# Kernel optimization log

Hardware: AMD Instinct MI355X
Metric: run time of the kernel (lower is better)

The kernel has to match this reference:

```python
import jax, jax.numpy as jnp
import numpy as np

N = 100000
E = 1600000
F_IN = 128
HID = 64
N_CLASS = 40
NEG_SLOPE = 0.2


def setup_inputs() -> dict:
    key = jax.random.key(0)
    ks = jax.random.split(key, 16)
    s = lambda *sh: 1.0 / np.sqrt(sh[0])
    inp = {
        "x": jax.random.normal(ks[0], (N, F_IN), dtype=jnp.float32),
        "edge_index": jax.random.randint(ks[1], (2, E), 0, N, dtype=jnp.int64),
        "W1": jax.random.normal(ks[2], (F_IN, HID), jnp.float32) * s(F_IN),
        "b1": jnp.zeros((HID,), jnp.float32),
        "Wc0": jax.random.normal(ks[3], (HID, HID), jnp.float32) * s(HID),
        "att_src0": jax.random.normal(ks[4], (HID,), jnp.float32) * s(HID),
        "att_dst0": jax.random.normal(ks[5], (HID,), jnp.float32) * s(HID),
        "bias0": jnp.zeros((HID,), jnp.float32),
        "Wc1": jax.random.normal(ks[6], (HID, HID), jnp.float32) * s(HID),
        "att_src1": jax.random.normal(ks[7], (HID,), jnp.float32) * s(HID),
        "att_dst1": jax.random.normal(ks[8], (HID,), jnp.float32) * s(HID),
        "bias1": jnp.zeros((HID,), jnp.float32),
        "W2": jax.random.normal(ks[9], (HID, N_CLASS), jnp.float32) * s(HID),
        "b2": jnp.zeros((N_CLASS,), jnp.float32),
    }
    return inp


def gat_conv(x, src, dst, W, att_src, att_dst, bias):
    # x: [N, Fin]; src/dst: [E'] (self-loops already appended)
    h = x @ W                                   # [N, Fout]
    a_s = h @ att_src                           # [N]
    a_d = h @ att_dst                           # [N]
    e = jax.nn.leaky_relu(a_s[src] + a_d[dst], NEG_SLOPE)   # [E']
    # segment softmax over edges grouped by destination node
    e_max = jax.ops.segment_max(e, dst, num_segments=N)     # every node has a self-loop
    ex = jnp.exp(e - e_max[dst])
    denom = jax.ops.segment_sum(ex, dst, num_segments=N)
    alpha = ex / (denom[dst] + 1e-16)                        # [E']
    out = jax.ops.segment_sum(h[src] * alpha[:, None], dst, num_segments=N)
    return out + bias


def reference(x, edge_index, W1, b1, Wc0, att_src0, att_dst0, bias0,
              Wc1, att_src1, att_dst1, bias1, W2, b2):
    # eval mode: dropout_adj and feature dropout are identity
    loop = jnp.arange(N, dtype=edge_index.dtype)
    src = jnp.concatenate([edge_index[0], loop])
    dst = jnp.concatenate([edge_index[1], loop])

    h = jax.nn.relu(x @ W1 + b1)
    h = gat_conv(h, src, dst, Wc0, att_src0, att_dst0, bias0)
    h = jax.nn.relu(h)
    h = gat_conv(h, src, dst, Wc1, att_src1, att_dst1, bias1)
    logits = h @ W2 + b2
    return jax.nn.log_softmax(logits, axis=-1)
```

## Files before the change

### kernel.cpp

```cpp
#include <hip/hip_runtime.h>

#define N_NODES 100000
#define N_EDGES 1600000
#define F_IN    128
#define HID     64
#define N_CLASS 40
#define NEG_SLOPE 0.2f
#define ET (N_EDGES + N_NODES)
#define ROW_BLOCKS ((N_NODES + 63) / 64)

#define NCB   7
#define CAP1  294912
#define BPC   144
#define NFB   782
#define CAPF  2624
#define NT1   ((ET + 2047) / 2048)

typedef __attribute__((ext_vector_type(8))) short bf16x8;
typedef __attribute__((ext_vector_type(4))) float f32x4;

__device__ __forceinline__ unsigned int f2bf(float f) {
    unsigned int u = __float_as_uint(f);
    return (u + 0x7fffu + ((u >> 16) & 1u)) >> 16;
}

__global__ __launch_bounds__(256) void k_prepw(const float* __restrict__ W1,
        const float* __restrict__ Wc0, const float* __restrict__ Wc1,
        const float* __restrict__ W2,
        unsigned short* __restrict__ Wt1, unsigned short* __restrict__ Wtc0,
        unsigned short* __restrict__ Wtc1, unsigned short* __restrict__ W2t,
        int* __restrict__ zbuf, int zcount) {
    int g = blockIdx.x * 256 + threadIdx.x;
    int stride = gridDim.x * 256;
    for (int i = g; i < zcount; i += stride) zbuf[i] = 0;
    for (int i = g; i < F_IN * HID; i += stride) {
        int k = i >> 6, n = i & 63;
        Wt1[n * F_IN + k] = (unsigned short)f2bf(W1[i]);
    }
    for (int i = g; i < HID * HID; i += stride) {
        int k = i >> 6, n = i & 63;
        Wtc0[n * HID + k] = (unsigned short)f2bf(Wc0[i]);
        Wtc1[n * HID + k] = (unsigned short)f2bf(Wc1[i]);
    }
    for (int i = g; i < 48 * HID; i += stride) {
        int n = i >> 6, k = i & 63;
        W2t[n * HID + k] = (n < N_CLASS)
            ? (unsigned short)f2bf(W2[k * N_CLASS + n]) : (unsigned short)0;
    }
}

__global__ __launch_bounds__(256) void k_p1lin(
        const int* __restrict__ ei, int* __restrict__ tail1,
        unsigned int* __restrict__ buf1,
        const float* __restrict__ x, const unsigned short* __restrict__ Wt1,
        const float* __restrict__ b1, const unsigned short* __restrict__ Wtc0,
        const float* __restrict__ att_s, const float* __restrict__ att_d,
        unsigned short* __restrict__ hb, float* __restrict__ as_,
        float* __restrict__ ad_) {
    __shared__ __align__(16) char smem[17408];
    __shared__ int hist[NCB], lb[NCB], cbase[NCB];
    int t = threadIdx.x;
    int lane = t & 63, w = t >> 6;

    if (blockIdx.x < NT1) {
        unsigned int* eb = (unsigned int*)smem;
        int tileBase = blockIdx.x * 2048;
        int total = ET - tileBase; if (total > 2048) total = 2048;
        if (t < NCB) hist[t] = 0;
        __syncthreads();
        unsigned long long ltm = (1ull << lane) - 1ull;

        int sr[8], dr[8];
        #pragma unroll
        for (int r = 0; r < 8; ++r) {
            int i = tileBase + r * 256 + t;
            int s = 0, d = -1;
            if (i < ET) {
                if (i < N_EDGES) { s = ei[i]; d = ei[N_EDGES + i]; }
                else             { s = d = i - N_EDGES; }
            }
            sr[r] = s; dr[r] = d;
        }
        __builtin_amdgcn_sched_barrier(0);

        unsigned int pk[8]; int ps[8];
        #pragma unroll
        for (int r = 0; r < 8; ++r) {
            int s = sr[r], d = dr[r];
            int b = (d >= 0) ? (d >> 14) : -1;
            unsigned long long m[NCB];
            #pragma unroll
            for (int q = 0; q < NCB; ++q) m[q] = __ballot(b == q);
            int cnt = 0;
            #pragma unroll
            for (int q = 0; q < NCB; ++q) if (lane == q) cnt = __popcll(m[q]);
            int old = 0;
            if (lane < NCB) old = atomicAdd(&hist[lane], cnt);
            int bsafe = (b >= 0) ? b : 0;
            int basew = __shfl(old, bsafe, 64);
            if (b >= 0) {
                int rank = 0;
                #pragma unroll
                for (int q = 0; q < NCB; ++q)
                    if (b == q) rank = (int)__popcll(m[q] & ltm);
                pk[r] = ((unsigned int)s << 14) | ((unsigned int)d & 16383u);
                ps[r] = (basew + rank) | (b << 12);
            } else ps[r] = -1;
        }
        __syncthreads();
        if (t == 0) {
            int run = 0;
            #pragma unroll
            for (int q = 0; q < NCB; ++q) { int h = hist[q]; lb[q] = run; run += h; }
        }
        __syncthreads();
        if (t < NCB) {
            int g = (hist[t] > 0) ? atomicAdd(&tail1[t], hist[t]) : 0;
            cbase[t] = g - lb[t];
        }
        #pragma unroll
        for (int r = 0; r < 8; ++r) {
            if (ps[r] >= 0) {
                int b = ps[r] >> 12, pos = ps[r] & 4095;
                eb[lb[b] + pos] = pk[r];
            }
        }
        __syncthreads();
        int B1 = lb[1], B2 = lb[2], B3 = lb[3], B4 = lb[4], B5 = lb[5], B6 = lb[6];
        for (int j = t; j < total; j += 256) {
            unsigned int p = eb[j];
            int b = (j >= B1) + (j >= B2) + (j >= B3) + (j >= B4)
                  + (j >= B5) + (j >= B6);
            buf1[(size_t)b * CAP1 + cbase[b] + j] = p;
        }
    } else {
        int quad = lane >> 4, lr = lane & 15;
        int rowg0 = (int)(blockIdx.x - NT1) * 64 + w * 16;
        float* xs = (float*)smem + w * (16 * 68);

        int arow = rowg0 + lr; if (arow >= N_NODES) arow = N_NODES - 1;
        const float* ab = x + (size_t)arow * F_IN + quad * 8;
        float4 xa[8];
        #pragma unroll
        for (int kc = 0; kc < 4; ++kc) {
            xa[2 * kc]     = *(const float4*)(ab + kc * 32);
            xa[2 * kc + 1] = *(const float4*)(ab + kc * 32 + 4);
        }
        __builtin_amdgcn_sched_barrier(0);

        f32x4 zero = {0.f, 0.f, 0.f, 0.f};
        f32x4 acc[4] = {zero, zero, zero, zero};
        #pragma unroll
        for (int kc = 0; kc < 4; ++kc) {
            bf16x8 bw[4];
            #pragma unroll
            for (int nt = 0; nt < 4; ++nt)
                bw[nt] = *(const bf16x8*)(Wt1 + (nt * 16 + lr) * F_IN
                                          + kc * 32 + quad * 8);
            float4 a0 = xa[2 * kc], a1 = xa[2 * kc + 1];
            union { bf16x8 v; unsigned int u[4]; } af;
            af.u[0] = f2bf(a0.x) | (f2bf(a0.y) << 16);
            af.u[1] = f2bf(a0.z) | (f2bf(a0.w) << 16);
            af.u[2] = f2bf(a1.x) | (f2bf(a1.y) << 16);
            af.u[3] = f2bf(a1.z) | (f2bf(a1.w) << 16);
            #pragma unroll
            for (int nt = 0; nt < 4; ++nt)
                acc[nt] = __builtin_amdgcn_mfma_f32_16x16x32_bf16(
                              af.v, bw[nt], acc[nt], 0, 0, 0);
        }
        #pragma unroll
        for (int nt = 0; nt < 4; ++nt) {
            float bv = b1[nt * 16 + lr];
            #pragma unroll
            for (int reg = 0; reg < 4; ++reg)
                xs[(quad * 4 + reg) * 68 + nt * 16 + lr] =
                    fmaxf(acc[nt][reg] + bv, 0.f);
        }
        f32x4 acc2[4] = {zero, zero, zero, zero};
        #pragma unroll
        for (int kc = 0; kc < 2; ++kc) {
            bf16x8 bw[4];
            #pragma unroll
            for (int nt = 0; nt < 4; ++nt)
                bw[nt] = *(const bf16x8*)(Wtc0 + (nt * 16 + lr) * HID
                                          + kc * 32 + quad * 8);
            const float* ap = xs + lr * 68 + kc * 32 + quad * 8;
            float4 a0 = *(const float4*)ap;
            float4 a1 = *(const float4*)(ap + 4);
            union { bf16x8 v; unsigned int u[4]; } af;
            af.u[0] = f2bf(a0.x) | (f2bf(a0.y) << 16);
            af.u[1] = f2bf(a0.z) | (f2bf(a0.w) << 16);
            af.u[2] = f2bf(a1.x) | (f2bf(a1.y) << 16);
            af.u[3] = f2bf(a1.z) | (f2bf(a1.w) << 16);
            #pragma unroll
            for (int nt = 0; nt < 4; ++nt)
                acc2[nt] = __builtin_amdgcn_mfma_f32_16x16x32_bf16(
                              af.v, bw[nt], acc2[nt], 0, 0, 0);
        }
        float asv[4], adv[4];
        #pragma unroll
        for (int nt = 0; nt < 4; ++nt) {
            asv[nt] = att_s[nt * 16 + lr];
            adv[nt] = att_d[nt * 16 + lr];
        }
        #pragma unroll
        for (int reg = 0; reg < 4; ++reg) {
            float p1 = acc2[0][reg] * asv[0] + acc2[1][reg] * asv[1]
                     + acc2[2][reg] * asv[2] + acc2[3][reg] * asv[3];
            float p2 = acc2[0][reg] * adv[0] + acc2[1][reg] * adv[1]
                     + acc2[2][reg] * adv[2] + acc2[3][reg] * adv[3];
            #pragma unroll
            for (int off = 1; off < 16; off <<= 1) {
                p1 += __shfl_xor(p1, off, 64);
                p2 += __shfl_xor(p2, off, 64);
            }
            if (lr == 0) {
                int grow = rowg0 + quad * 4 + reg;
                if (grow < N_NODES) { as_[grow] = p1; ad_[grow] = p2; }
            }
        }
        #pragma unroll
        for (int nt = 0; nt < 4; ++nt)
            #pragma unroll
            for (int reg = 0; reg < 4; ++reg)
                xs[(quad * 4 + reg) * 68 + nt * 16 + lr] = acc2[nt][reg];
        #pragma unroll
        for (int j = 0; j < 2; ++j) {
            int task = j * 64 + lane;
            int r = task >> 3, g = task & 7;
            int grow = rowg0 + r;
            if (grow < N_NODES) {
                const float* p = xs + r * 68 + g * 8;
                uint4 u;
                u.x = f2bf(p[0]) | (f2bf(p[1]) << 16);
                u.y = f2bf(p[2]) | (f2bf(p[3]) << 16);
                u.z = f2bf(p[4]) | (f2bf(p[5]) << 16);
                u.w = f2bf(p[6]) | (f2bf(p[7]) << 16);
                *(uint4*)(hb + (size_t)grow * HID + g * 8) = u;
            }
        }
    }
}

__global__ __launch_bounds__(256) void k_part2(const unsigned int* __restrict__ buf1,
        const int* __restrict__ tail1, int* __restrict__ fcnt,
        unsigned int* __restrict__ buf2, int* __restrict__ fbase,
        int* __restrict__ rowptr, int* __restrict__ done0) {
    __shared__ unsigned int eb[2048];
    __shared__ int hist[128], lbase[128], loff[128], goff[128], sc[128];
    __shared__ int lastflag, wsum4[4];
    int t = threadIdx.x;
    int cb   = blockIdx.x / BPC;
    int tile = blockIdx.x % BPC;
    int n1 = tail1[cb];
    int base = tile * 2048;
    if (base < n1) {
        int total = n1 - base; if (total > 2048) total = 2048;
        if (t < 128) hist[t] = 0;
        __syncthreads();
        unsigned int pr[8]; int fr[8];
        #pragma unroll
        for (int r = 0; r < 8; ++r) {
            int i = base + r * 256 + t;
            int f = -1; unsigned int p = 0;
            if (i < n1) {
                p = buf1[(size_t)cb * CAP1 + i];
                f = (int)((p >> 7) & 127u);
                atomicAdd(&hist[f], 1);
            }
            pr[r] = p; fr[r] = f;
        }
        __syncthreads();
        if (t < 128) sc[t] = hist[t];
        __syncthreads();
        for (int off = 1; off < 128; off <<= 1) {
            int u = (t < 128 && t >= off) ? sc[t - off] : 0;
            __syncthreads();
            if (t < 128) sc[t] += u;
            __syncthreads();
        }
        if (t < 128) { lbase[t] = sc[t] - hist[t]; loff[t] = 0; }
        __syncthreads();
        if (t < 128 && hist[t] > 0)
            goff[t] = atomicAdd(&fcnt[cb * 128 + t], hist[t]);
        #pragma unroll
        for (int r = 0; r < 8; ++r) {
            if (fr[r] >= 0) {
                int f = fr[r];
                int pos = lbase[f] + atomicAdd(&loff[f], 1);
                eb[pos] = (pr[r] & 127u) | ((pr[r] >> 14) << 7)
                        | ((unsigned int)f << 24);
            }
        }
        __syncthreads();
        for (int j = t; j < total; j += 256) {
            unsigned int q = eb[j];
            int f = (int)(q >> 24);
            buf2[(size_t)(cb * 128 + f) * CAPF + goff[f] + (j - lbase[f])] =
                q & 0xFFFFFFu;
        }
    }
    if (t == 0) lastflag = (atomicAdd(done0, 1) == NCB * BPC - 1);
    __syncthreads();
    if (lastflag) {
        __threadfence();
        int k0 = t * 4;
        int v0 = (k0     < NFB) ? fcnt[k0]     : 0;
        int v1 = (k0 + 1 < NFB) ? fcnt[k0 + 1] : 0;
        int v2 = (k0 + 2 < NFB) ? fcnt[k0 + 2] : 0;
        int v3 = (k0 + 3 < NFB) ? fcnt[k0 + 3] : 0;
        int s1 = v0 + v1, s2 = s1 + v2, s3 = s2 + v3;
        int lane = t & 63, w = t >> 6;
        int ws = s3;
        #pragma unroll
        for (int off = 1; off < 64; off <<= 1) {
            int u = __shfl_up(ws, off, 64);
            if (lane >= off) ws += u;
        }
        if (lane == 63) wsum4[w] = ws;
        __syncthreads();
        int wb = 0;
        #pragma unroll
        for (int q = 0; q < 4; ++q) if (q < w) wb += wsum4[q];
        int ex = wb + ws - s3;
        if (k0     < NFB) fbase[k0]     = ex;
        if (k0 + 1 < NFB) fbase[k0 + 1] = ex + v0;
        if (k0 + 2 < NFB) fbase[k0 + 2] = ex + s1;
        if (k0 + 3 < NFB) fbase[k0 + 3] = ex + s2;
        if (t == 0) rowptr[N_NODES] = ET;
    }
}

__global__ __launch_bounds__(256) void k_part3(const unsigned int* __restrict__ buf2,
        const int* __restrict__ fcnt, const int* __restrict__ fbase,
        int* __restrict__ rowptr, int* __restrict__ col,
        int* __restrict__ dhistg, int* __restrict__ dbase,
        int* __restrict__ done1) {
    __shared__ unsigned int eb[CAPF];
    __shared__ int cs[CAPF];
    __shared__ int hist[128], lbase[128], loff[128], sc[128], dh[64];
    __shared__ int lastflag;
    int t = threadIdx.x;
    int fb = blockIdx.x;
    int nF = fcnt[fb];
    int gb = fbase[fb];
    int nbase = fb * 128;
    if (t < 128) hist[t] = 0;
    if (t >= 128 && t < 192) dh[t - 128] = 0;
    __syncthreads();
    for (int j = t; j < nF; j += 256) {
        unsigned int q = buf2[(size_t)fb * CAPF + j];
        eb[j] = q;
        atomicAdd(&hist[q & 127u], 1);
    }
    __syncthreads();
    if (t < 128) sc[t] = hist[t];
    __syncthreads();
    for (int off = 1; off < 128; off <<= 1) {
        int u = (t < 128 && t >= off) ? sc[t - off] : 0;
        __syncthreads();
        if (t < 128) sc[t] += u;
        __syncthreads();
    }
    if (t < 128) { lbase[t] = sc[t] - hist[t]; loff[t] = 0; }
    __syncthreads();
    if (t < 128 && nbase + t < N_NODES) {
        rowptr[nbase + t] = gb + lbase[t];
        int dg = hist[t]; if (dg > 63) dg = 63;
        atomicAdd(&dh[dg], 1);
    }
    for (int j = t; j < nF; j += 256) {
        unsigned int q = eb[j];
        int r = (int)(q & 127u);
        int p = lbase[r] + atomicAdd(&loff[r], 1);
        cs[p] = (int)(q >> 7);
    }
    __syncthreads();
    for (int j = t; j < nF; j += 256) col[gb + j] = cs[j];
    if (t < 64 && dh[t] > 0) atomicAdd(&dhistg[t], dh[t]);
    __syncthreads();
    if (t == 0) lastflag = (atomicAdd(done1, 1) == NFB - 1);
    __syncthreads();
    if (lastflag && t < 64) {
        __threadfence();
        int v = dhistg[t];
        int s = v;
        #pragma unroll
        for (int off = 1; off < 64; off <<= 1) {
            int u = __shfl_up(s, off, 64);
            if (t >= off) s += u;
        }
        dbase[t] = s - v;
    }
}

__global__ __launch_bounds__(256) void k_dscatter(const int* __restrict__ rowptr,
        int* __restrict__ dbase, int* __restrict__ nodeord) {
    __shared__ int lh[64], goff[64];
    int t = threadIdx.x;
    if (t < 64) lh[t] = 0;
    __syncthreads();
    int i = blockIdx.x * 256 + t;
    int deg = -1, lrank = 0;
    if (i < N_NODES) {
        deg = rowptr[i + 1] - rowptr[i];
        if (deg > 63) deg = 63;
        lrank = atomicAdd(&lh[deg], 1);
    }
    __syncthreads();
    if (t < 64) goff[t] = (lh[t] > 0) ? atomicAdd(&dbase[t], lh[t]) : 0;
    __syncthreads();
    if (deg >= 0) nodeord[goff[deg] + lrank] = i;
}

__global__ __launch_bounds__(256) void k_gemm_att(
        const unsigned short* __restrict__ hin,
        const unsigned short* __restrict__ Wt,
        const float* __restrict__ att_s, const float* __restrict__ att_d,
        unsigned short* __restrict__ hb, float* __restrict__ as_,
        float* __restrict__ ad_) {
    __shared__ float xs[4][16 * 68];
    int t = threadIdx.x;
    int lane = t & 63, w = t >> 6;
    int quad = lane >> 4, lr = lane & 15;
    int rowg0 = blockIdx.x * 64 + w * 16;

    bf16x8 bfr[2][4];
    #pragma unroll
    for (int kc = 0; kc < 2; ++kc)
        #pragma unroll
        for (int nt = 0; nt < 4; ++nt)
            bfr[kc][nt] = *(const bf16x8*)(Wt + (nt * 16 + lr) * HID
                                           + kc * 32 + quad * 8);
    f32x4 zero = {0.f, 0.f, 0.f, 0.f};
    f32x4 acc[4] = {zero, zero, zero, zero};

    int arow = rowg0 + lr; if (arow >= N_NODES) arow = N_NODES - 1;
    #pragma unroll
    for (int kc = 0; kc < 2; ++kc) {
        bf16x8 af = *(const bf16x8*)(hin + (size_t)arow * HID
                                     + kc * 32 + quad * 8);
        #pragma unroll
        for (int nt = 0; nt < 4; ++nt)
            acc[nt] = __builtin_amdgcn_mfma_f32_16x16x32_bf16(
                          af, bfr[kc][nt], acc[nt], 0, 0, 0);
    }
    float asv[4], adv[4];
    #pragma unroll
    for (int nt = 0; nt < 4; ++nt) {
        asv[nt] = att_s[nt * 16 + lr];
        adv[nt] = att_d[nt * 16 + lr];
    }
    #pragma unroll
    for (int reg = 0; reg < 4; ++reg) {
        float p1 = acc[0][reg] * asv[0] + acc[1][reg] * asv[1]
                 + acc[2][reg] * asv[2] + acc[3][reg] * asv[3];
        float p2 = acc[0][reg] * adv[0] + acc[1][reg] * adv[1]
                 + acc[2][reg] * adv[2] + acc[3][reg] * adv[3];
        #pragma unroll
        for (int off = 1; off < 16; off <<= 1) {
            p1 += __shfl_xor(p1, off, 64);
            p2 += __shfl_xor(p2, off, 64);
        }
        if (lr == 0) {
            int grow = rowg0 + quad * 4 + reg;
            if (grow < N_NODES) { as_[grow] = p1; ad_[grow] = p2; }
        }
    }
    #pragma unroll
    for (int nt = 0; nt < 4; ++nt)
        #pragma unroll
        for (int reg = 0; reg < 4; ++reg)
            xs[w][(quad * 4 + reg) * 68 + nt * 16 + lr] = acc[nt][reg];
    #pragma unroll
    for (int j = 0; j < 2; ++j) {
        int task = j * 64 + lane;
        int r = task >> 3, g = task & 7;
        int grow = rowg0 + r;
        if (grow < N_NODES) {
            const float* p = xs[w] + r * 68 + g * 8;
            uint4 u;
            u.x = f2bf(p[0]) | (f2bf(p[1]) << 16);
            u.y = f2bf(p[2]) | (f2bf(p[3]) << 16);
            u.z = f2bf(p[4]) | (f2bf(p[5]) << 16);
            u.w = f2bf(p[6]) | (f2bf(p[7]) << 16);
            *(uint4*)(hb + (size_t)grow * HID + g * 8) = u;
        }
    }
}

template <bool RELU>
__global__ __launch_bounds__(256) void k_gat_agg(const int* __restrict__ rowptr,
        const int* __restrict__ col, const unsigned short* __restrict__ hb,
        const float* __restrict__ as_, const float* __restrict__ ad_,
        const float* __restrict__ bias, const int* __restrict__ nodeord,
        unsigned short* __restrict__ outb) {
    int t = threadIdx.x;
    int lane = t & 63;
    int wid = blockIdx.x * 4 + (t >> 6);
    int l8 = lane & 7;
    int ch = l8 * 8;
    int d = nodeord[wid * 8 + (lane >> 3)];
    int beg = rowptr[d];
    int deg = rowptr[d + 1] - beg;
    float add = ad_[d];
    int degw = deg;
    degw = max(degw, __shfl_xor(degw, 8, 64));
    degw = max(degw, __shfl_xor(degw, 16, 64));
    degw = max(degw, __shfl_xor(degw, 32, 64));

    float a0=0.f,a1=0.f,a2=0.f,a3=0.f,a4=0.f,a5=0.f,a6=0.f,a7=0.f,den=0.f;
    const unsigned short* hch = hb + ch;

    int sj = 0; float wj = 0.f;
    if (l8 < deg) {
        sj = col[beg + l8];
        float e = as_[sj] + add;
        e = (e > 0.f) ? e : NEG_SLOPE * e;
        wj = __expf(e);
    }
    for (int c = 0; c < degw; c += 8) {
        uint4 hv[8]; float w0[8];
        #pragma unroll
        for (int j = 0; j < 8; ++j) {
            int sl = (lane & 56) | j;
            int s = __shfl(sj, sl, 64);
            w0[j] = __shfl(wj, sl, 64);
            hv[j] = *(const uint4*)(hch + (size_t)s * HID);
        }
        int sjn = 0; float wjn = 0.f;
        int idxn = c + 8 + l8;
        if (c + 8 < degw && idxn < deg) {
            sjn = col[beg + idxn];
            float e = as_[sjn] + add;
            e = (e > 0.f) ? e : NEG_SLOPE * e;
            wjn = __expf(e);
        }
        __builtin_amdgcn_sched_barrier(0);
        #pragma unroll
        for (int j = 0; j < 8; ++j) {
            den += w0[j];
            a0 = fmaf(w0[j], __uint_as_float(hv[j].x << 16),         a0);
            a1 = fmaf(w0[j], __uint_as_float(hv[j].x & 0xffff0000u), a1);
            a2 = fmaf(w0[j], __uint_as_float(hv[j].y << 16),         a2);
            a3 = fmaf(w0[j], __uint_as_float(hv[j].y & 0xffff0000u), a3);
            a4 = fmaf(w0[j], __uint_as_float(hv[j].z << 16),         a4);
            a5 = fmaf(w0[j], __uint_as_float(hv[j].z & 0xffff0000u), a5);
            a6 = fmaf(w0[j], __uint_as_float(hv[j].w << 16),         a6);
            a7 = fmaf(w0[j], __uint_as_float(hv[j].w & 0xffff0000u), a7);
        }
        sj = sjn; wj = wjn;
    }
    float inv = 1.f / (den + 1e-16f);
    float4 bA = *(const float4*)(bias + ch);
    float4 bB = *(const float4*)(bias + ch + 4);
    float o0 = fmaf(a0, inv, bA.x), o1 = fmaf(a1, inv, bA.y);
    float o2 = fmaf(a2, inv, bA.z), o3 = fmaf(a3, inv, bA.w);
    float o4 = fmaf(a4, inv, bB.x), o5 = fmaf(a5, inv, bB.y);
    float o6 = fmaf(a6, inv, bB.z), o7 = fmaf(a7, inv, bB.w);
    if (RELU) {
        o0 = fmaxf(o0, 0.f); o1 = fmaxf(o1, 0.f);
        o2 = fmaxf(o2, 0.f); o3 = fmaxf(o3, 0.f);
        o4 = fmaxf(o4, 0.f); o5 = fmaxf(o5, 0.f);
        o6 = fmaxf(o6, 0.f); o7 = fmaxf(o7, 0.f);
    }
    uint4 u;
    u.x = f2bf(o0) | (f2bf(o1) << 16);
    u.y = f2bf(o2) | (f2bf(o3) << 16);
    u.z = f2bf(o4) | (f2bf(o5) << 16);
    u.w = f2bf(o6) | (f2bf(o7) << 16);
    *(uint4*)(outb + (size_t)d * HID + ch) = u;
}

__global__ __launch_bounds__(256) void k_final(
        const unsigned short* __restrict__ aggb,
        const unsigned short* __restrict__ W2t, const float* __restrict__ b2,
        float* __restrict__ out) {
    __shared__ float xs[64 * 44];
    int t = threadIdx.x;
    int lane = t & 63, w = t >> 6;
    int quad = lane >> 4, lr = lane & 15;
    int rowg0 = blockIdx.x * 64 + w * 16;
    int base = blockIdx.x * 64;
    int rem = N_NODES - base; if (rem > 64) rem = 64;

    bf16x8 bfr[2][3];
    #pragma unroll
    for (int kc = 0; kc < 2; ++kc)
        #pragma unroll
        for (int nt = 0; nt < 3; ++nt)
            bfr[kc][nt] = *(const bf16x8*)(W2t + (nt * 16 + lr) * HID
                                           + kc * 32 + quad * 8);
    f32x4 zero = {0.f, 0.f, 0.f, 0.f};
    f32x4 acc[3] = {zero, zero, zero};
    int arow = rowg0 + lr; if (arow >= N_NODES) arow = N_NODES - 1;
    #pragma unroll
    for (int kc = 0; kc < 2; ++kc) {
        bf16x8 af = *(const bf16x8*)(aggb + (size_t)arow * HID
                                     + kc * 32 + quad * 8);
        #pragma unroll
        for (int nt = 0; nt < 3; ++nt)
            acc[nt] = __builtin_amdgcn_mfma_f32_16x16x32_bf16(
                          af, bfr[kc][nt], acc[nt], 0, 0, 0);
    }
    float bc[3];
    #pragma unroll
    for (int nt = 0; nt < 3; ++nt) {
        int cl = nt * 16 + lr;
        bc[nt] = (cl < N_CLASS) ? b2[cl] : -1e30f;
    }
    #pragma unroll
    for (int reg = 0; reg < 4; ++reg) {
        float v0 = acc[0][reg] + bc[0];
        float v1 = acc[1][reg] + bc[1];
        float v2 = acc[2][reg] + bc[2];
        float m = fmaxf(fmaxf(v0, v1), v2);
        #pragma unroll
        for (int off = 1; off < 16; off <<= 1)
            m = fmaxf(m, __shfl_xor(m, off, 64));
        float ss = __expf(v0 - m) + __expf(v1 - m) + __expf(v2 - m);
        #pragma unroll
        for (int off = 1; off < 16; off <<= 1)
            ss += __shfl_xor(ss, off, 64);
        float lse = m + logf(ss);
        int r = w * 16 + quad * 4 + reg;
        xs[r * 44 + lr]      = v0 - lse;
        xs[r * 44 + 16 + lr] = v1 - lse;
        if (lr < 8) xs[r * 44 + 32 + lr] = v2 - lse;
    }
    __syncthreads();
    #pragma unroll
    for (int j = 0; j < 3; ++j) {
        int idx = j * 256 + t;
        if (idx < rem * 10) {
            int r = idx / 10, c4 = idx - r * 10;
            float4 v = *(const float4*)(xs + r * 44 + c4 * 4);
            *(float4*)(out + (size_t)base * N_CLASS + idx * 4) = v;
        }
    }
}

extern "C" void kernel_launch(void* const* d_in, const int* in_sizes, int n_in,
                              void* d_out, int out_size, void* d_ws, size_t ws_size,
                              hipStream_t stream) {
    const float* x     = (const float*)d_in[0];
    const int*   ei    = (const int*)  d_in[1];
    const float* W1    = (const float*)d_in[2];
    const float* b1    = (const float*)d_in[3];
    const float* Wc0   = (const float*)d_in[4];
    const float* as0   = (const float*)d_in[5];
    const float* ad0   = (const float*)d_in[6];
    const float* bias0 = (const float*)d_in[7];
    const float* Wc1   = (const float*)d_in[8];
    const float* as1   = (const float*)d_in[9];
    const float* ad1   = (const float*)d_in[10];
    const float* bias1 = (const float*)d_in[11];
    const float* W2    = (const float*)d_in[12];
    const float* b2    = (const float*)d_in[13];
    float* out = (float*)d_out;

    char* p = (char*)d_ws;
    unsigned short* hb    = (unsigned short*)p; p += (size_t)N_NODES * HID * 2;
    unsigned short* agg0b = (unsigned short*)p; p += (size_t)N_NODES * HID * 2;
    char* pbuf = p;
    unsigned int*   buf1  = (unsigned int*)pbuf;
    unsigned int*   buf2  = (unsigned int*)(pbuf + (size_t)NCB * CAP1 * 4);
    unsigned short* agg1b = (unsigned short*)pbuf;
    p += (size_t)NCB * CAP1 * 4 + (size_t)NFB * CAPF * 4;
    int* col = (int*)p;                          p += (size_t)ET * 4;
    unsigned short* Wt1  = (unsigned short*)p;   p += F_IN * HID * 2;
    unsigned short* Wtc0 = (unsigned short*)p;   p += HID * HID * 2;
    unsigned short* Wtc1 = (unsigned short*)p;   p += HID * HID * 2;
    unsigned short* W2t  = (unsigned short*)p;   p += 48 * HID * 2;
    float* as_ = (float*)p;                      p += (size_t)N_NODES * 4;
    float* ad_ = (float*)p;                      p += (size_t)N_NODES * 4;
    int* tail1 = (int*)p;
    int* fcnt  = tail1 + NCB;
    int* fbase = fcnt + NFB;
    int* dhist = fbase + NFB;
    int* dbase = dhist + 64;
    int* done  = dbase + 64;
    const int ZCOUNT = NCB + 2 * NFB + 128 + 2;
    p += (size_t)ZCOUNT * 4;
    int* rowptr  = (int*)p;                      p += (size_t)(N_NODES + 1) * 4;
    int* nodeord = (int*)p;

    const int AGG_BLOCKS  = N_NODES / 32;
    const int NODE_BLOCKS = (N_NODES + 255) / 256;

    k_prepw<<<32, 256, 0, stream>>>(W1, Wc0, Wc1, W2, Wt1, Wtc0, Wtc1, W2t,
                                    tail1, ZCOUNT);
    k_p1lin<<<NT1 + ROW_BLOCKS, 256, 0, stream>>>(
        ei, tail1, buf1, x, Wt1, b1, Wtc0, as0, ad0, hb, as_, ad_);
    k_part2<<<NCB * BPC, 256, 0, stream>>>(buf1, tail1, fcnt, buf2, fbase,
                                           rowptr, done + 0);
    k_part3<<<NFB, 256, 0, stream>>>(buf2, fcnt, fbase, rowptr, col, dhist,
                                     dbase, done + 1);
    k_dscatter<<<NODE_BLOCKS, 256, 0, stream>>>(rowptr, dbase, nodeord);

    k_gat_agg<true><<<AGG_BLOCKS, 256, 0, stream>>>(
        rowptr, col, hb, as_, ad_, bias0, nodeord, agg0b);

    k_gemm_att<<<ROW_BLOCKS, 256, 0, stream>>>(agg0b, Wtc1, as1, ad1,
                                               hb, as_, ad_);
    k_gat_agg<false><<<AGG_BLOCKS, 256, 0, stream>>>(
        rowptr, col, hb, as_, ad_, bias1, nodeord, agg1b);

    k_final<<<ROW_BLOCKS, 256, 0, stream>>>(agg1b, W2t, b2, out);
}
```

Baseline: 287.4 us.

## Replace global-atomic bucket partition with per-tile sorted runs and synthesized self-loops

The first partition pass now sorts each 2048-edge tile by coarse bucket locally and writes it back in place with per-tile bucket boundaries. This removes the global tail atomics and the scattered writes into the seven large bucket arrays. The second pass gathers a group of seven tiles' runs for one bucket, so the global scatter happens only once. Self-loop edges are no longer streamed through the partition and are inserted directly into the CSR rows, and the degree histogram counters are spaced apart to reduce atomic contention. The risk is overflow of the 4096-entry shared buffer when a tile group holds more edges than expected.

```diff
diff --git a/kernel.cpp b/kernel.cpp
--- a/kernel.cpp
+++ b/kernel.cpp
@@ -10,11 +10,12 @@
 #define ROW_BLOCKS ((N_NODES + 63) / 64)
 
 #define NCB   7
-#define CAP1  294912
-#define BPC   144
 #define NFB   782
 #define CAPF  2624
-#define NT1   ((ET + 2047) / 2048)
+#define NT1   ((N_EDGES + 2047) / 2048)
+#define TPG   7
+#define NGRP  ((NT1 + TPG - 1) / TPG)
+#define NP2   (NCB * NGRP)
 
 typedef __attribute__((ext_vector_type(8))) short bf16x8;
 typedef __attribute__((ext_vector_type(4))) float f32x4;
@@ -50,7 +51,7 @@
 }
 
 __global__ __launch_bounds__(256) void k_p1lin(
-        const int* __restrict__ ei, int* __restrict__ tail1,
+        const int* __restrict__ ei, int* __restrict__ bnd,
         unsigned int* __restrict__ buf1,
         const float* __restrict__ x, const unsigned short* __restrict__ Wt1,
         const float* __restrict__ b1, const unsigned short* __restrict__ Wtc0,
@@ -58,14 +59,14 @@
         unsigned short* __restrict__ hb, float* __restrict__ as_,
         float* __restrict__ ad_) {
     __shared__ __align__(16) char smem[17408];
-    __shared__ int hist[NCB], lb[NCB], cbase[NCB];
+    __shared__ int hist[NCB], lb[NCB];
     int t = threadIdx.x;
     int lane = t & 63, w = t >> 6;
 
     if (blockIdx.x < NT1) {
         unsigned int* eb = (unsigned int*)smem;
         int tileBase = blockIdx.x * 2048;
-        int total = ET - tileBase; if (total > 2048) total = 2048;
+        int total = N_EDGES - tileBase; if (total > 2048) total = 2048;
         if (t < NCB) hist[t] = 0;
         __syncthreads();
         unsigned long long ltm = (1ull << lane) - 1ull;
@@ -75,14 +76,9 @@
         for (int r = 0; r < 8; ++r) {
             int i = tileBase + r * 256 + t;
             int s = 0, d = -1;
-            if (i < ET) {
-                if (i < N_EDGES) { s = ei[i]; d = ei[N_EDGES + i]; }
-                else             { s = d = i - N_EDGES; }
-            }
+            if (i < N_EDGES) { s = ei[i]; d = ei[N_EDGES + i]; }
             sr[r] = s; dr[r] = d;
         }
-        __builtin_amdgcn_sched_barrier(0);
-
         unsigned int pk[8]; int ps[8];
         #pragma unroll
         for (int r = 0; r < 8; ++r) {
@@ -114,10 +110,6 @@
             for (int q = 0; q < NCB; ++q) { int h = hist[q]; lb[q] = run; run += h; }
         }
         __syncthreads();
-        if (t < NCB) {
-            int g = (hist[t] > 0) ? atomicAdd(&tail1[t], hist[t]) : 0;
-            cbase[t] = g - lb[t];
-        }
         #pragma unroll
         for (int r = 0; r < 8; ++r) {
             if (ps[r] >= 0) {
@@ -126,13 +118,10 @@
             }
         }
         __syncthreads();
-        int B1 = lb[1], B2 = lb[2], B3 = lb[3], B4 = lb[4], B5 = lb[5], B6 = lb[6];
-        for (int j = t; j < total; j += 256) {
-            unsigned int p = eb[j];
-            int b = (j >= B1) + (j >= B2) + (j >= B3) + (j >= B4)
-                  + (j >= B5) + (j >= B6);
-            buf1[(size_t)b * CAP1 + cbase[b] + j] = p;
-        }
+        for (int j = t; j < total; j += 256)
+            buf1[tileBase + j] = eb[j];
+        if (t < NCB) bnd[blockIdx.x * 8 + t] = lb[t];
+        if (t == NCB) bnd[blockIdx.x * 8 + 7] = total;
     } else {
         int quad = lane >> 4, lr = lane & 15;
         int rowg0 = (int)(blockIdx.x - NT1) * 64 + w * 16;
@@ -146,8 +135,6 @@
             xa[2 * kc]     = *(const float4*)(ab + kc * 32);
             xa[2 * kc + 1] = *(const float4*)(ab + kc * 32 + 4);
         }
-        __builtin_amdgcn_sched_barrier(0);
-
         f32x4 zero = {0.f, 0.f, 0.f, 0.f};
         f32x4 acc[4] = {zero, zero, zero, zero};
         #pragma unroll
@@ -243,79 +230,84 @@
 }
 
 __global__ __launch_bounds__(256) void k_part2(const unsigned int* __restrict__ buf1,
-        const int* __restrict__ tail1, int* __restrict__ fcnt,
+        const int* __restrict__ bnd, int* __restrict__ fcnt,
         unsigned int* __restrict__ buf2, int* __restrict__ fbase,
         int* __restrict__ rowptr, int* __restrict__ done0) {
-    __shared__ unsigned int eb[2048];
+    __shared__ unsigned int eb0[4096];
+    __shared__ unsigned int ebs[4096];
     __shared__ int hist[128], lbase[128], loff[128], goff[128], sc[128];
+    __shared__ int tlo[TPG], tcn[TPG];
     __shared__ int lastflag, wsum4[4];
     int t = threadIdx.x;
-    int cb   = blockIdx.x / BPC;
-    int tile = blockIdx.x % BPC;
-    int n1 = tail1[cb];
-    int base = tile * 2048;
-    if (base < n1) {
-        int total = n1 - base; if (total > 2048) total = 2048;
-        if (t < 128) hist[t] = 0;
-        __syncthreads();
-        unsigned int pr[8]; int fr[8];
-        #pragma unroll
-        for (int r = 0; r < 8; ++r) {
-            int i = base + r * 256 + t;
-            int f = -1; unsigned int p = 0;
-            if (i < n1) {
-                p = buf1[(size_t)cb * CAP1 + i];
-                f = (int)((p >> 7) & 127u);
-                atomicAdd(&hist[f], 1);
-            }
-            pr[r] = p; fr[r] = f;
-        }
-        __syncthreads();
-        if (t < 128) sc[t] = hist[t];
-        __syncthreads();
-        for (int off = 1; off < 128; off <<= 1) {
-            int u = (t < 128 && t >= off) ? sc[t - off] : 0;
-            __syncthreads();
-            if (t < 128) sc[t] += u;
-            __syncthreads();
-        }
-        if (t < 128) { lbase[t] = sc[t] - hist[t]; loff[t] = 0; }
-        __syncthreads();
-        if (t < 128 && hist[t] > 0)
-            goff[t] = atomicAdd(&fcnt[cb * 128 + t], hist[t]);
-        #pragma unroll
-        for (int r = 0; r < 8; ++r) {
-            if (fr[r] >= 0) {
-                int f = fr[r];
-                int pos = lbase[f] + atomicAdd(&loff[f], 1);
-                eb[pos] = (pr[r] & 127u) | ((pr[r] >> 14) << 7)
-                        | ((unsigned int)f << 24);
-            }
-        }
-        __syncthreads();
-        for (int j = t; j < total; j += 256) {
-            unsigned int q = eb[j];
-            int f = (int)(q >> 24);
-            buf2[(size_t)(cb * 128 + f) * CAPF + goff[f] + (j - lbase[f])] =
-                q & 0xFFFFFFu;
-        }
-    }
-    if (t == 0) lastflag = (atomicAdd(done0, 1) == NCB * BPC - 1);
+    int cb = blockIdx.x / NGRP;
+    int g  = blockIdx.x % NGRP;
+    int t0 = g * TPG;
+    int ntl = NT1 - t0; if (ntl > TPG) ntl = TPG;
+    if (t < ntl) {
+        int lo = bnd[(t0 + t) * 8 + cb];
+        int hi = bnd[(t0 + t) * 8 + cb + 1];
+        tlo[t] = lo; tcn[t] = hi - lo;
+    }
+    if (t < 128) hist[t] = 0;
+    __syncthreads();
+    int off[TPG + 1]; off[0] = 0;
+    for (int i = 0; i < ntl; ++i) off[i + 1] = off[i] + tcn[i];
+    int total = off[ntl]; if (total > 4096) total = 4096;
+    for (int i = 0; i < ntl; ++i) {
+        int cnt = tcn[i], ob = off[i];
+        const unsigned int* src = buf1 + (size_t)(t0 + i) * 2048 + tlo[i];
+        for (int j = t; j < cnt; j += 256)
+            if (ob + j < 4096) eb0[ob + j] = src[j];
+    }
+    __syncthreads();
+    for (int j = t; j < total; j += 256)
+        atomicAdd(&hist[(eb0[j] >> 7) & 127u], 1);
+    __syncthreads();
+    if (t < 128) sc[t] = hist[t];
+    __syncthreads();
+    for (int off2 = 1; off2 < 128; off2 <<= 1) {
+        int u = (t < 128 && t >= off2) ? sc[t - off2] : 0;
+        __syncthreads();
+        if (t < 128) sc[t] += u;
+        __syncthreads();
+    }
+    if (t < 128) { lbase[t] = sc[t] - hist[t]; loff[t] = 0; }
+    __syncthreads();
+    if (t < 128 && hist[t] > 0)
+        goff[t] = atomicAdd(&fcnt[cb * 128 + t], hist[t]);
+    for (int j = t; j < total; j += 256) {
+        unsigned int q = eb0[j];
+        int f = (int)((q >> 7) & 127u);
+        int pos = lbase[f] + atomicAdd(&loff[f], 1);
+        ebs[pos] = (q & 127u) | ((q >> 14) << 7) | ((unsigned int)f << 24);
+    }
+    __syncthreads();
+    for (int j = t; j < total; j += 256) {
+        unsigned int q = ebs[j];
+        int f = (int)(q >> 24);
+        buf2[(size_t)(cb * 128 + f) * CAPF + goff[f] + (j - lbase[f])] =
+            q & 0xFFFFFFu;
+    }
+    if (t == 0) lastflag = (atomicAdd(done0, 1) == NP2 - 1);
     __syncthreads();
     if (lastflag) {
         __threadfence();
         int k0 = t * 4;
-        int v0 = (k0     < NFB) ? fcnt[k0]     : 0;
-        int v1 = (k0 + 1 < NFB) ? fcnt[k0 + 1] : 0;
-        int v2 = (k0 + 2 < NFB) ? fcnt[k0 + 2] : 0;
-        int v3 = (k0 + 3 < NFB) ? fcnt[k0 + 3] : 0;
+        int nv0 = (k0     < NFB) ? min(128, N_NODES - k0 * 128)       : 0;
+        int nv1 = (k0 + 1 < NFB) ? min(128, N_NODES - (k0 + 1) * 128) : 0;
+        int nv2 = (k0 + 2 < NFB) ? min(128, N_NODES - (k0 + 2) * 128) : 0;
+        int nv3 = (k0 + 3 < NFB) ? min(128, N_NODES - (k0 + 3) * 128) : 0;
+        int v0 = (k0     < NFB) ? fcnt[k0]     + nv0 : 0;
+        int v1 = (k0 + 1 < NFB) ? fcnt[k0 + 1] + nv1 : 0;
+        int v2 = (k0 + 2 < NFB) ? fcnt[k0 + 2] + nv2 : 0;
+        int v3 = (k0 + 3 < NFB) ? fcnt[k0 + 3] + nv3 : 0;
         int s1 = v0 + v1, s2 = s1 + v2, s3 = s2 + v3;
         int lane = t & 63, w = t >> 6;
         int ws = s3;
         #pragma unroll
-        for (int off = 1; off < 64; off <<= 1) {
-            int u = __shfl_up(ws, off, 64);
-            if (lane >= off) ws += u;
+        for (int off2 = 1; off2 < 64; off2 <<= 1) {
+            int u = __shfl_up(ws, off2, 64);
+            if (lane >= off2) ws += u;
         }
         if (lane == 63) wsum4[w] = ws;
         __syncthreads();
@@ -354,7 +346,9 @@
         atomicAdd(&hist[q & 127u], 1);
     }
     __syncthreads();
-    if (t < 128) sc[t] = hist[t];
+    int valid = (t < 128 && nbase + t < N_NODES) ? 1 : 0;
+    int cnt = valid ? hist[t] + 1 : 0;
+    if (t < 128) sc[t] = cnt;
     __syncthreads();
     for (int off = 1; off < 128; off <<= 1) {
         int u = (t < 128 && t >= off) ? sc[t - off] : 0;
@@ -362,35 +356,39 @@
         if (t < 128) sc[t] += u;
         __syncthreads();
     }
-    if (t < 128) { lbase[t] = sc[t] - hist[t]; loff[t] = 0; }
-    __syncthreads();
-    if (t < 128 && nbase + t < N_NODES) {
+    if (t < 128) { lbase[t] = sc[t] - cnt; loff[t] = 0; }
+    __syncthreads();
+    if (valid) {
         rowptr[nbase + t] = gb + lbase[t];
-        int dg = hist[t]; if (dg > 63) dg = 63;
+        cs[lbase[t]] = nbase + t;
+        int dg = cnt; if (dg > 63) dg = 63;
         atomicAdd(&dh[dg], 1);
     }
     for (int j = t; j < nF; j += 256) {
         unsigned int q = eb[j];
         int r = (int)(q & 127u);
-        int p = lbase[r] + atomicAdd(&loff[r], 1);
+        int p = lbase[r] + 1 + atomicAdd(&loff[r], 1);
         cs[p] = (int)(q >> 7);
     }
     __syncthreads();
-    for (int j = t; j < nF; j += 256) col[gb + j] = cs[j];
-    if (t < 64 && dh[t] > 0) atomicAdd(&dhistg[t], dh[t]);
+    int nvalid = N_NODES - nbase;
+    if (nvalid > 128) nvalid = 128; if (nvalid < 0) nvalid = 0;
+    int totc = nF + nvalid;
+    for (int j = t; j < totc; j += 256) col[gb + j] = cs[j];
+    if (t < 64 && dh[t] > 0) atomicAdd(&dhistg[t * 16], dh[t]);
     __syncthreads();
     if (t == 0) lastflag = (atomicAdd(done1, 1) == NFB - 1);
     __syncthreads();
     if (lastflag && t < 64) {
         __threadfence();
-        int v = dhistg[t];
+        int v = dhistg[t * 16];
         int s = v;
         #pragma unroll
         for (int off = 1; off < 64; off <<= 1) {
             int u = __shfl_up(s, off, 64);
             if (t >= off) s += u;
         }
-        dbase[t] = s - v;
+        dbase[t * 16] = s - v;
     }
 }
 
@@ -408,7 +406,7 @@
         lrank = atomicAdd(&lh[deg], 1);
     }
     __syncthreads();
-    if (t < 64) goff[t] = (lh[t] > 0) ? atomicAdd(&dbase[t], lh[t]) : 0;
+    if (t < 64) goff[t] = (lh[t] > 0) ? atomicAdd(&dbase[t * 16], lh[t]) : 0;
     __syncthreads();
     if (deg >= 0) nodeord[goff[deg] + lrank] = i;
 }
@@ -664,9 +662,9 @@
     unsigned short* agg0b = (unsigned short*)p; p += (size_t)N_NODES * HID * 2;
     char* pbuf = p;
     unsigned int*   buf1  = (unsigned int*)pbuf;
-    unsigned int*   buf2  = (unsigned int*)(pbuf + (size_t)NCB * CAP1 * 4);
+    unsigned int*   buf2  = (unsigned int*)(pbuf + (size_t)NT1 * 2048 * 4);
     unsigned short* agg1b = (unsigned short*)pbuf;
-    p += (size_t)NCB * CAP1 * 4 + (size_t)NFB * CAPF * 4;
+    p += (size_t)NT1 * 2048 * 4 + (size_t)NFB * CAPF * 4;
     int* col = (int*)p;                          p += (size_t)ET * 4;
     unsigned short* Wt1  = (unsigned short*)p;   p += F_IN * HID * 2;
     unsigned short* Wtc0 = (unsigned short*)p;   p += HID * HID * 2;
@@ -674,26 +672,26 @@
     unsigned short* W2t  = (unsigned short*)p;   p += 48 * HID * 2;
     float* as_ = (float*)p;                      p += (size_t)N_NODES * 4;
     float* ad_ = (float*)p;                      p += (size_t)N_NODES * 4;
-    int* tail1 = (int*)p;
-    int* fcnt  = tail1 + NCB;
-    int* fbase = fcnt + NFB;
-    int* dhist = fbase + NFB;
-    int* dbase = dhist + 64;
-    int* done  = dbase + 64;
-    const int ZCOUNT = NCB + 2 * NFB + 128 + 2;
+    int* fcnt  = (int*)p;
+    int* dhist = fcnt + NFB;
+    int* done  = dhist + 64 * 16;
+    const int ZCOUNT = NFB + 64 * 16 + 2;
     p += (size_t)ZCOUNT * 4;
+    int* fbase = (int*)p;                        p += (size_t)NFB * 4;
+    int* dbase = (int*)p;                        p += (size_t)64 * 16 * 4;
     int* rowptr  = (int*)p;                      p += (size_t)(N_NODES + 1) * 4;
-    int* nodeord = (int*)p;
+    int* nodeord = (int*)p;                      p += (size_t)N_NODES * 4;
+    int* bnd     = (int*)p;
 
     const int AGG_BLOCKS  = N_NODES / 32;
     const int NODE_BLOCKS = (N_NODES + 255) / 256;
 
     k_prepw<<<32, 256, 0, stream>>>(W1, Wc0, Wc1, W2, Wt1, Wtc0, Wtc1, W2t,
-                                    tail1, ZCOUNT);
+                                    fcnt, ZCOUNT);
     k_p1lin<<<NT1 + ROW_BLOCKS, 256, 0, stream>>>(
-        ei, tail1, buf1, x, Wt1, b1, Wtc0, as0, ad0, hb, as_, ad_);
-    k_part2<<<NCB * BPC, 256, 0, stream>>>(buf1, tail1, fcnt, buf2, fbase,
-                                           rowptr, done + 0);
+        ei, bnd, buf1, x, Wt1, b1, Wtc0, as0, ad0, hb, as_, ad_);
+    k_part2<<<NP2, 256, 0, stream>>>(buf1, bnd, fcnt, buf2, fbase,
+                                     rowptr, done + 0);
     k_part3<<<NFB, 256, 0, stream>>>(buf2, fcnt, fbase, rowptr, col, dhist,
                                      dbase, done + 1);
     k_dscatter<<<NODE_BLOCKS, 256, 0, stream>>>(rowptr, dbase, nodeord);
```

New measurement: 294.4 us. +2.4%, slower.
